# Kernel optimization log

Measured on AMD Instinct MI355X. Metric: run time of the kernel, lower is better.

## Reference

```python
import jax, jax.numpy as jnp
import numpy as np

B, L, D, H, S = 4, 4096, 1024, 16, 4
DH = D // H


def setup_inputs() -> dict:
    key = jax.random.key(0)
    ks = jax.random.split(key, 12)
    std = 0.02
    inp = {
        "x": jax.random.normal(ks[0], (B, L, D), jnp.float32),
        "scale_logits": jax.random.normal(ks[1], (S,), jnp.float32),
        "wq": jax.random.normal(ks[2], (D, D), jnp.float32) * std,
        "bq": jnp.zeros((D,), jnp.float32),
        "wk": jax.random.normal(ks[3], (D, D), jnp.float32) * std,
        "bk": jnp.zeros((D,), jnp.float32),
        "wv": jax.random.normal(ks[4], (D, D), jnp.float32) * std,
        "bv": jnp.zeros((D,), jnp.float32),
        "wo": jax.random.normal(ks[5], (D, D), jnp.float32) * std,
        "bo": jnp.zeros((D,), jnp.float32),
        "ws": jax.random.normal(ks[6], (S, D, D), jnp.float32) * std,  # per-scale Linear weights (out,in)
        "bs": jax.random.normal(ks[7], (S, D), jnp.float32) * std,
    }
    return inp


def reference(x, scale_logits, wq, bq, wk, bk, wv, bv, wo, bo, ws, bs):
    # q/k/v projections; kept flat (B,L,D) since the torch code re-flattens before scale proj
    qf = x @ wq.T + bq
    kf = x @ wk.T + bk
    vf = x @ wv.T + bv
    # per-scale linear projection, vectorized over scales: (B,S,L,D)
    sq = jnp.einsum('bld,sed->bsle', qf, ws) + bs[None, :, None, :]
    sk = jnp.einsum('bld,sed->bsle', kf, ws) + bs[None, :, None, :]
    sv = jnp.einsum('bld,sed->bsle', vf, ws) + bs[None, :, None, :]
    sq = sq.reshape(B, S, L, H, DH)
    sk = sk.reshape(B, S, L, H, DH)
    sv = sv.reshape(B, S, L, H, DH)
    # faithful to torch: matmul over last two dims of (B,L,H,dh) -> per-position
    # head-mixing scores of shape (B,S,L,H,H)
    scale = 1.0 / np.sqrt(DH).astype(np.float32)
    scores = jnp.einsum('bslhd,bslgd->bslhg', sq, sk) * scale
    attn = jax.nn.softmax(scores, axis=-1)
    out = jnp.einsum('bslhg,bslgd->bslhd', attn, sv)  # (B,S,L,H,DH)
    w = jax.nn.softmax(scale_logits, axis=0)  # (S,)
    combined = jnp.einsum('s,bslhd->blhd', w, out).reshape(B, L, D)
    return combined @ wo.T + bo
```

## Files before the change

kernel.cpp:

```cpp
#include <hip/hip_runtime.h>


typedef unsigned short u16;
typedef __attribute__((ext_vector_type(8))) short s16x8;
typedef __attribute__((ext_vector_type(8))) unsigned short u16x8;
typedef __attribute__((ext_vector_type(4))) float f32x4;

#define MM 16384
#define DDIM 1024
#define DDSQ 1048576ull

__device__ __forceinline__ u16 f2bf(float f) {
  unsigned u = __float_as_uint(f);
  u = (u + 0x7FFFu + ((u >> 16) & 1u)) >> 16;
  return (u16)u;
}
__device__ __forceinline__ float b2f(u16 b) {
  return __uint_as_float(((unsigned)b) << 16);
}
__device__ __forceinline__ void gload_lds16(const void* g, void* l) {
  __builtin_amdgcn_global_load_lds(
      (const __attribute__((address_space(1))) void*)g,
      (__attribute__((address_space(3))) void*)l, 16, 0, 0);
}

__global__ __launch_bounds__(256) void k_f32_to_bf16(
    const float* __restrict__ in, u16* __restrict__ out, int n4) {
  int i = blockIdx.x * 256 + threadIdx.x;
  if (i >= n4) return;
  float4 v = reinterpret_cast<const float4*>(in)[i];
  ushort4 o;
  o.x = f2bf(v.x); o.y = f2bf(v.y); o.z = f2bf(v.z); o.w = f2bf(v.w);
  reinterpret_cast<ushort4*>(out)[i] = o;
}

__global__ __launch_bounds__(256) void k_transpose_bf16(
    const float* __restrict__ wq, const float* __restrict__ wk,
    const float* __restrict__ wv, u16* __restrict__ out) {
  __shared__ float tile[32][33];
  const float* src = (blockIdx.z == 0) ? wq : (blockIdx.z == 1) ? wk : wv;
  u16* dst = out + (size_t)blockIdx.z * DDSQ;
  int tx = threadIdx.x, ty = threadIdx.y;
  int bx = blockIdx.x * 32, by = blockIdx.y * 32;
#pragma unroll
  for (int i = 0; i < 4; ++i)
    tile[ty + 8 * i][tx] = src[(size_t)(by + ty + 8 * i) * DDIM + bx + tx];
  __syncthreads();
#pragma unroll
  for (int i = 0; i < 4; ++i)
    dst[(size_t)(bx + ty + 8 * i) * DDIM + by + tx] = f2bf(tile[tx][ty + 8 * i]);
}

__global__ __launch_bounds__(256) void k_bias_fuse(
    const float* __restrict__ ws, const float* __restrict__ bq,
    const float* __restrict__ bk, const float* __restrict__ bv,
    const float* __restrict__ bs, float* __restrict__ bf) {
  int idx = blockIdx.y;
  int s = idx / 3, t = idx - s * 3;
  const float* bt = (t == 0) ? bq : (t == 1) ? bk : bv;
  int lane = threadIdx.x & 63, wid = threadIdx.x >> 6;
  int e = blockIdx.x * 4 + wid;
  const float* wr = ws + (size_t)s * DDSQ + (size_t)e * DDIM;
  float p = 0.f;
  for (int j = lane; j < DDIM; j += 64) p += wr[j] * bt[j];
#pragma unroll
  for (int off = 32; off > 0; off >>= 1) p += __shfl_xor(p, off);
  if (lane == 0) bf[idx * DDIM + e] = p + bs[s * DDIM + e];
}

template <typename OutT>
__global__ __launch_bounds__(256) void k_gemm_bt(
    const u16* __restrict__ A, const u16* __restrict__ B, OutT* __restrict__ C,
    const float* __restrict__ bias, int M, int N, int K,
    size_t za, size_t zb, size_t zc, size_t zbias, int zmode) {
  __shared__ u16 lds_a[128 * 32];
  __shared__ u16 lds_b[128 * 32];

  int z = blockIdx.x >> 3;
  int n_blk = blockIdx.x & 7;
  int m_blk = blockIdx.y;
  if (zmode == 1) { A += (size_t)(z / 3) * za; B += (size_t)(z % 3) * zb; }
  else            { A += (size_t)z * za;       B += (size_t)z * zb; }
  C += (size_t)z * zc;
  const float* biasz = bias ? (bias + (size_t)z * zbias) : nullptr;

  int m0 = m_blk * 128, n0 = n_blk * 128;
  int tid = threadIdx.x;
  int lane = tid & 63, wid = tid >> 6;
  int wm = wid >> 1, wn = wid & 1;

  f32x4 acc[4][4] = {};

  auto stage = [&](int k0) {
#pragma unroll
    for (int i = 0; i < 2; ++i) {
      int c = wid * 2 + i;
      int row = c * 16 + (lane >> 2);
      int col = (lane & 3) * 8;
      gload_lds16(A + (size_t)(m0 + row) * K + k0 + col, &lds_a[c * 512]);
      gload_lds16(B + (size_t)(n0 + row) * K + k0 + col, &lds_b[c * 512]);
    }
  };

  stage(0);
  int ar = (wm * 64 + (lane & 15)) * 32 + (lane >> 4) * 8;
  int br = (wn * 64 + (lane & 15)) * 32 + (lane >> 4) * 8;
  for (int k0 = 0;;) {
    __syncthreads();
    s16x8 af[4], bfr[4];
#pragma unroll
    for (int mi = 0; mi < 4; ++mi)
      af[mi] = *reinterpret_cast<const s16x8*>(&lds_a[ar + mi * 16 * 32]);
#pragma unroll
    for (int ni = 0; ni < 4; ++ni)
      bfr[ni] = *reinterpret_cast<const s16x8*>(&lds_b[br + ni * 16 * 32]);
#pragma unroll
    for (int mi = 0; mi < 4; ++mi)
#pragma unroll
      for (int ni = 0; ni < 4; ++ni)
        acc[mi][ni] = __builtin_amdgcn_mfma_f32_16x16x32_bf16(
            af[mi], bfr[ni], acc[mi][ni], 0, 0, 0);
    k0 += 32;
    if (k0 >= K) break;
    __syncthreads();
    stage(k0);
  }

#pragma unroll
  for (int mi = 0; mi < 4; ++mi) {
#pragma unroll
    for (int ni = 0; ni < 4; ++ni) {
      int colg = n0 + wn * 64 + ni * 16 + (lane & 15);
      float badd = biasz ? biasz[colg] : 0.f;
#pragma unroll
      for (int r = 0; r < 4; ++r) {
        int rowg = m0 + wm * 64 + mi * 16 + ((lane >> 4) << 2) + r;
        float v = acc[mi][ni][r] + badd;
        if constexpr (sizeof(OutT) == 2) C[(size_t)rowg * N + colg] = f2bf(v);
        else                             C[(size_t)rowg * N + colg] = v;
      }
    }
  }
}

template <typename OutT>
__global__ __launch_bounds__(512, 1) void k_gemm256(
    const u16* __restrict__ A, const u16* __restrict__ B, OutT* __restrict__ C,
    const float* __restrict__ bias, int M, int N, int K,
    size_t za, size_t zb, size_t zc, size_t zbias, int nbx) {
  __shared__ u16 lds[4][2][8192];

  int z = blockIdx.x / nbx;
  int nb = blockIdx.x - z * nbx;
  const u16* Ag = A + (size_t)z * za;
  const u16* Bg = B + (size_t)z * zb;
  OutT* Cg = C + (size_t)z * zc;
  const float* biasz = bias + (size_t)z * zbias;

  int m0 = blockIdx.y * 256, n0 = nb * 256;
  int tid = threadIdx.x;
  int lane = tid & 63, wid = tid >> 6;
  int wm = wid >> 2, wn = wid & 3;
  int NT = K >> 5;

  int scb = ((lane & 3) * 16) ^ (((lane >> 3) & 3) << 4);
  const char* srcA[2]; const char* srcB[2]; int ldsc[2];
#pragma unroll
  for (int r = 0; r < 2; ++r) {
    int c = r * 8 + wid;
    int row = c * 16 + (lane >> 2);
    srcA[r] = (const char*)Ag + ((size_t)(m0 + row) * K) * 2 + scb;
    srcB[r] = (const char*)Bg + ((size_t)(n0 + row) * K) * 2 + scb;
    ldsc[r] = c * 1024;
  }
  char* lbase = (char*)&lds[0][0][0];

  int fxor = ((lane >> 4) * 16) ^ (((lane >> 1) & 3) << 4);
  int aoff = (wm * 128 + (lane & 15)) * 64 + fxor;
  int boff = (wn * 64 + (lane & 15)) * 64 + fxor;

  f32x4 acc[8][4] = {};
  s16x8 cA0[4], cA1[4], cB[4];
  s16x8 nA0[4], nA1[4], nB[4];

#define STAGE_A(kt, rg)                                                   \
  {                                                                       \
    _Pragma("unroll") for (int r = 0; r < 2; ++r)                         \
        gload_lds16(srcA[r] + (size_t)(kt) * 64,                          \
                    lbase + (rg) * 32768 + ldsc[r]);                      \
  }
#define STAGE_B(kt, rg)                                                   \
  {                                                                       \
    _Pragma("unroll") for (int r = 0; r < 2; ++r)                         \
        gload_lds16(srcB[r] + (size_t)(kt) * 64,                          \
                    lbase + (rg) * 32768 + 16384 + ldsc[r]);              \
  }

#define SUBITER(C0, C1, CBv, N0, N1, NBv, tcur)                           \
  {                                                                       \
    asm volatile("s_waitcnt vmcnt(4)" ::: "memory");                      \
    asm volatile("s_barrier" ::: "memory");                               \
    int tn = (tcur) + 1 < NT ? (tcur) + 1 : NT - 1;                       \
    const char* bA = lbase + (tn & 3) * 32768;                            \
    const char* bB = bA + 16384;                                          \
    _Pragma("unroll") for (int i = 0; i < 4; ++i)                         \
        NBv[i] = *(const s16x8*)(bB + boff + i * 1024);                   \
    _Pragma("unroll") for (int i = 0; i < 4; ++i)                         \
        N0[i] = *(const s16x8*)(bA + aoff + i * 1024);                    \
    _Pragma("unroll") for (int i = 0; i < 4; ++i)                         \
        N1[i] = *(const s16x8*)(bA + aoff + 4096 + i * 1024);             \
    int ts = (tcur) + 3 < NT ? (tcur) + 3 : NT - 1;                       \
    int rgs = ((tcur) + 3) & 3;                                           \
    STAGE_A(ts, rgs); STAGE_B(ts, rgs);                                   \
    __builtin_amdgcn_s_setprio(1);                                        \
    _Pragma("unroll") for (int mi = 0; mi < 4; ++mi)                      \
      _Pragma("unroll") for (int ni = 0; ni < 4; ++ni)                    \
          acc[mi][ni] = __builtin_amdgcn_mfma_f32_16x16x32_bf16(          \
              C0[mi], CBv[ni], acc[mi][ni], 0, 0, 0);                     \
    _Pragma("unroll") for (int mi = 0; mi < 4; ++mi)                      \
      _Pragma("unroll") for (int ni = 0; ni < 4; ++ni)                    \
          acc[mi + 4][ni] = __builtin_amdgcn_mfma_f32_16x16x32_bf16(      \
              C1[mi], CBv[ni], acc[mi + 4][ni], 0, 0, 0);                 \
    __builtin_amdgcn_s_setprio(0);                                        \
  }

  STAGE_A(0, 0); STAGE_B(0, 0);
  STAGE_A(1, 1); STAGE_B(1, 1);
  STAGE_A(2, 2); STAGE_B(2, 2);
  asm volatile("s_waitcnt vmcnt(8)" ::: "memory");
  asm volatile("s_barrier" ::: "memory");
  {
    const char* bA = lbase;
    const char* bB = bA + 16384;
#pragma unroll
    for (int i = 0; i < 4; ++i) cB[i]  = *(const s16x8*)(bB + boff + i * 1024);
#pragma unroll
    for (int i = 0; i < 4; ++i) cA0[i] = *(const s16x8*)(bA + aoff + i * 1024);
#pragma unroll
    for (int i = 0; i < 4; ++i)
      cA1[i] = *(const s16x8*)(bA + aoff + 4096 + i * 1024);
  }

  for (int t = 0; t < NT; t += 2) {
    SUBITER(cA0, cA1, cB, nA0, nA1, nB, t);
    SUBITER(nA0, nA1, nB, cA0, cA1, cB, t + 1);
  }
#undef SUBITER
#undef STAGE_A
#undef STAGE_B

  asm volatile("s_waitcnt vmcnt(0)" ::: "memory");

#pragma unroll
  for (int mi = 0; mi < 8; ++mi) {
#pragma unroll
    for (int ni = 0; ni < 4; ++ni) {
      int colg = n0 + wn * 64 + ni * 16 + (lane & 15);
      float badd = biasz[colg];
#pragma unroll
      for (int r = 0; r < 4; ++r) {
        int rowg = m0 + wm * 128 + mi * 16 + ((lane >> 4) << 2) + r;
        float v = acc[mi][ni][r] + badd;
        if constexpr (sizeof(OutT) == 2) Cg[(size_t)rowg * N + colg] = f2bf(v);
        else                             Cg[(size_t)rowg * N + colg] = v;
      }
    }
  }
}

__global__ __launch_bounds__(256) void k_attn_all(
    const u16* __restrict__ proj, u16* __restrict__ outbf,
    const float* __restrict__ sl, int rows) {
  __shared__ u16 kv[4][2][1024];
  int lane = threadIdx.x & 63, wid = threadIdx.x >> 6;
  int row = blockIdx.x * 4 + wid;
  int h = lane >> 2, dq = lane & 3;
  int doff = h * 64 + dq * 16;

  float l0 = sl[0], l1 = sl[1], l2 = sl[2], l3 = sl[3];
  float lm = fmaxf(fmaxf(l0, l1), fmaxf(l2, l3));
  float e0 = __expf(l0 - lm), e1 = __expf(l1 - lm), e2 = __expf(l2 - lm),
        e3 = __expf(l3 - lm);
  float esum = e0 + e1 + e2 + e3;
  float wsc4[4] = {e0 / esum, e1 / esum, e2 / esum, e3 / esum};

  float acc[16];
#pragma unroll
  for (int i = 0; i < 16; ++i) acc[i] = 0.f;

  for (int s = 0; s < 4; ++s) {
    const u16* kr = proj + ((size_t)(3 * s + 1) * rows + row) * DDIM;
    const u16* vr = proj + ((size_t)(3 * s + 2) * rows + row) * DDIM;
    asm volatile("s_waitcnt vmcnt(0) lgkmcnt(0)" ::: "memory");
    gload_lds16(kr + lane * 8,       &kv[wid][0][0]);
    gload_lds16(kr + 512 + lane * 8, &kv[wid][0][512]);
    gload_lds16(vr + lane * 8,       &kv[wid][1][0]);
    gload_lds16(vr + 512 + lane * 8, &kv[wid][1][512]);

    const u16* qr = proj + ((size_t)(3 * s) * rows + row) * DDIM + doff;
    u16x8 q0 = *reinterpret_cast<const u16x8*>(qr);
    u16x8 q1 = *reinterpret_cast<const u16x8*>(qr + 8);
    float qf[16];
#pragma unroll
    for (int i = 0; i < 8; ++i) {
      qf[i]     = b2f(q0[i]) * 0.125f;
      qf[8 + i] = b2f(q1[i]) * 0.125f;
    }
    asm volatile("s_waitcnt vmcnt(0)" ::: "memory");

    float sc[16];
#pragma unroll
    for (int g = 0; g < 16; ++g) {
      const u16* kp = &kv[wid][0][g * 64 + dq * 16];
      u16x8 k0 = *reinterpret_cast<const u16x8*>(kp);
      u16x8 k1 = *reinterpret_cast<const u16x8*>(kp + 8);
      float d = 0.f;
#pragma unroll
      for (int i = 0; i < 8; ++i) d = fmaf(qf[i], b2f(k0[i]), d);
#pragma unroll
      for (int i = 0; i < 8; ++i) d = fmaf(qf[8 + i], b2f(k1[i]), d);
      d += __shfl_xor(d, 1);
      d += __shfl_xor(d, 2);
      sc[g] = d;
    }

    float mx = sc[0];
#pragma unroll
    for (int g = 1; g < 16; ++g) mx = fmaxf(mx, sc[g]);
    float sum = 0.f;
#pragma unroll
    for (int g = 0; g < 16; ++g) { sc[g] = __expf(sc[g] - mx); sum += sc[g]; }
    float inv = wsc4[s] / sum;
#pragma unroll
    for (int g = 0; g < 16; ++g) sc[g] *= inv;

#pragma unroll
    for (int g = 0; g < 16; ++g) {
      float a = sc[g];
      const u16* vp = &kv[wid][1][g * 64 + dq * 16];
      u16x8 v0 = *reinterpret_cast<const u16x8*>(vp);
      u16x8 v1 = *reinterpret_cast<const u16x8*>(vp + 8);
#pragma unroll
      for (int i = 0; i < 8; ++i) {
        acc[i]     = fmaf(a, b2f(v0[i]), acc[i]);
        acc[8 + i] = fmaf(a, b2f(v1[i]), acc[8 + i]);
      }
    }
  }

  u16* op = outbf + (size_t)row * DDIM + doff;
  u16x8 o0, o1;
#pragma unroll
  for (int i = 0; i < 8; ++i) {
    o0[i] = f2bf(acc[i]);
    o1[i] = f2bf(acc[8 + i]);
  }
  *reinterpret_cast<u16x8*>(op) = o0;
  *reinterpret_cast<u16x8*>(op + 8) = o1;
}

extern "C" void kernel_launch(void* const* d_in, const int* in_sizes, int n_in,
                              void* d_out, int out_size, void* d_ws,
                              size_t ws_size, hipStream_t stream) {
  const float* x  = (const float*)d_in[0];
  const float* sl = (const float*)d_in[1];
  const float* wq = (const float*)d_in[2];
  const float* bq = (const float*)d_in[3];
  const float* wk = (const float*)d_in[4];
  const float* bk = (const float*)d_in[5];
  const float* wv = (const float*)d_in[6];
  const float* bv = (const float*)d_in[7];
  const float* wo = (const float*)d_in[8];
  const float* bo = (const float*)d_in[9];
  const float* ws = (const float*)d_in[10];
  const float* bs = (const float*)d_in[11];
  float* out = (float*)d_out;

  char* wsb = (char*)d_ws;
  size_t off = 0;
  u16* xbf    = (u16*)(wsb + off); off += (size_t)MM * DDIM * 2;
  u16* wfus   = (u16*)(wsb + off); off += 12ull * DDSQ * 2;
  u16* wobf   = (u16*)(wsb + off); off += DDSQ * 2;
  float* bfus = (float*)(wsb + off); off += 65536;
  u16* combc  = (u16*)(wsb + off); off += (size_t)MM * DDIM * 2;
  char* dynr  = wsb + off;
  size_t fixed = off;

  int chunk = 4096;
  while (chunk > 1024 && fixed + (size_t)12 * chunk * DDIM * 2 > ws_size)
    chunk >>= 1;
  u16* projc = (u16*)dynr;
  u16* wtT  = (u16*)dynr;
  u16* wsbf = (u16*)(dynr + 3ull * DDSQ * 2);

  int n4;
  n4 = MM * DDIM / 4;
  k_f32_to_bf16<<<(n4 + 255) / 256, 256, 0, stream>>>(x, xbf, n4);
  n4 = (int)(4 * DDSQ / 4);
  k_f32_to_bf16<<<(n4 + 255) / 256, 256, 0, stream>>>(ws, wsbf, n4);
  n4 = (int)(DDSQ / 4);
  k_f32_to_bf16<<<(n4 + 255) / 256, 256, 0, stream>>>(wo, wobf, n4);

  k_transpose_bf16<<<dim3(32, 32, 3), dim3(32, 8), 0, stream>>>(wq, wk, wv, wtT);
  k_bias_fuse<<<dim3(256, 12), 256, 0, stream>>>(ws, bq, bk, bv, bs, bfus);

  k_gemm_bt<u16><<<dim3(96, 8), 256, 0, stream>>>(
      wsbf, wtT, wfus, nullptr, 1024, 1024, 1024, DDSQ, DDSQ, DDSQ, 0, 1);

  int nchunks = MM / chunk;
  for (int c = 0; c < nchunks; ++c) {
    const u16* xa = xbf + (size_t)c * chunk * DDIM;
    k_gemm256<u16><<<dim3(48, chunk / 256), 512, 0, stream>>>(
        xa, wfus, projc, bfus, chunk, 1024, 1024,
        0, DDSQ, (size_t)chunk * DDIM, DDIM, 4);
    k_attn_all<<<dim3(chunk / 4), 256, 0, stream>>>(
        projc, combc + (size_t)c * chunk * DDIM, sl, chunk);
  }

  k_gemm256<float><<<dim3(4, 64), 512, 0, stream>>>(
      combc, wobf, out, bo, MM, 1024, 1024, 0, 0, 0, 0, 4);
}
```

Baseline: 717.9 us.

## Double-buffer QKV loads in attention, replace small GEMM, tune MFMA scheduling

The per-row attention kernel now stages q, k and v for two scales into a double-buffered LDS area and prefetches the next scales while computing the current one, instead of a full wait per scale with q read straight from global memory. The weight-fusion GEMM moves from the simple 128-tile kernel to the pipelined 256-tile kernel through a new zmode argument. In that kernel, s_setprio is replaced by sched_group_barrier hints that interleave MFMA, VMEM and LDS reads. The attention LDS footprint grows threefold, which may lower occupancy.

```diff
diff --git a/kernel.cpp b/kernel.cpp
--- a/kernel.cpp
+++ b/kernel.cpp
@@ -69,93 +69,19 @@
 }
 
 template <typename OutT>
-__global__ __launch_bounds__(256) void k_gemm_bt(
-    const u16* __restrict__ A, const u16* __restrict__ B, OutT* __restrict__ C,
-    const float* __restrict__ bias, int M, int N, int K,
-    size_t za, size_t zb, size_t zc, size_t zbias, int zmode) {
-  __shared__ u16 lds_a[128 * 32];
-  __shared__ u16 lds_b[128 * 32];
-
-  int z = blockIdx.x >> 3;
-  int n_blk = blockIdx.x & 7;
-  int m_blk = blockIdx.y;
-  if (zmode == 1) { A += (size_t)(z / 3) * za; B += (size_t)(z % 3) * zb; }
-  else            { A += (size_t)z * za;       B += (size_t)z * zb; }
-  C += (size_t)z * zc;
-  const float* biasz = bias ? (bias + (size_t)z * zbias) : nullptr;
-
-  int m0 = m_blk * 128, n0 = n_blk * 128;
-  int tid = threadIdx.x;
-  int lane = tid & 63, wid = tid >> 6;
-  int wm = wid >> 1, wn = wid & 1;
-
-  f32x4 acc[4][4] = {};
-
-  auto stage = [&](int k0) {
-#pragma unroll
-    for (int i = 0; i < 2; ++i) {
-      int c = wid * 2 + i;
-      int row = c * 16 + (lane >> 2);
-      int col = (lane & 3) * 8;
-      gload_lds16(A + (size_t)(m0 + row) * K + k0 + col, &lds_a[c * 512]);
-      gload_lds16(B + (size_t)(n0 + row) * K + k0 + col, &lds_b[c * 512]);
-    }
-  };
-
-  stage(0);
-  int ar = (wm * 64 + (lane & 15)) * 32 + (lane >> 4) * 8;
-  int br = (wn * 64 + (lane & 15)) * 32 + (lane >> 4) * 8;
-  for (int k0 = 0;;) {
-    __syncthreads();
-    s16x8 af[4], bfr[4];
-#pragma unroll
-    for (int mi = 0; mi < 4; ++mi)
-      af[mi] = *reinterpret_cast<const s16x8*>(&lds_a[ar + mi * 16 * 32]);
-#pragma unroll
-    for (int ni = 0; ni < 4; ++ni)
-      bfr[ni] = *reinterpret_cast<const s16x8*>(&lds_b[br + ni * 16 * 32]);
-#pragma unroll
-    for (int mi = 0; mi < 4; ++mi)
-#pragma unroll
-      for (int ni = 0; ni < 4; ++ni)
-        acc[mi][ni] = __builtin_amdgcn_mfma_f32_16x16x32_bf16(
-            af[mi], bfr[ni], acc[mi][ni], 0, 0, 0);
-    k0 += 32;
-    if (k0 >= K) break;
-    __syncthreads();
-    stage(k0);
-  }
-
-#pragma unroll
-  for (int mi = 0; mi < 4; ++mi) {
-#pragma unroll
-    for (int ni = 0; ni < 4; ++ni) {
-      int colg = n0 + wn * 64 + ni * 16 + (lane & 15);
-      float badd = biasz ? biasz[colg] : 0.f;
-#pragma unroll
-      for (int r = 0; r < 4; ++r) {
-        int rowg = m0 + wm * 64 + mi * 16 + ((lane >> 4) << 2) + r;
-        float v = acc[mi][ni][r] + badd;
-        if constexpr (sizeof(OutT) == 2) C[(size_t)rowg * N + colg] = f2bf(v);
-        else                             C[(size_t)rowg * N + colg] = v;
-      }
-    }
-  }
-}
-
-template <typename OutT>
 __global__ __launch_bounds__(512, 1) void k_gemm256(
     const u16* __restrict__ A, const u16* __restrict__ B, OutT* __restrict__ C,
     const float* __restrict__ bias, int M, int N, int K,
-    size_t za, size_t zb, size_t zc, size_t zbias, int nbx) {
+    size_t za, size_t zb, size_t zc, size_t zbias, int nbx, int zmode) {
   __shared__ u16 lds[4][2][8192];
 
   int z = blockIdx.x / nbx;
   int nb = blockIdx.x - z * nbx;
-  const u16* Ag = A + (size_t)z * za;
-  const u16* Bg = B + (size_t)z * zb;
+  const u16* Ag; const u16* Bg;
+  if (zmode == 1) { Ag = A + (size_t)(z / 3) * za; Bg = B + (size_t)(z % 3) * zb; }
+  else            { Ag = A + (size_t)z * za;       Bg = B + (size_t)z * zb; }
   OutT* Cg = C + (size_t)z * zc;
-  const float* biasz = bias + (size_t)z * zbias;
+  const float* biasz = bias ? (bias + (size_t)z * zbias) : nullptr;
 
   int m0 = blockIdx.y * 256, n0 = nb * 256;
   int tid = threadIdx.x;
@@ -212,7 +138,6 @@
     int ts = (tcur) + 3 < NT ? (tcur) + 3 : NT - 1;                       \
     int rgs = ((tcur) + 3) & 3;                                           \
     STAGE_A(ts, rgs); STAGE_B(ts, rgs);                                   \
-    __builtin_amdgcn_s_setprio(1);                                        \
     _Pragma("unroll") for (int mi = 0; mi < 4; ++mi)                      \
       _Pragma("unroll") for (int ni = 0; ni < 4; ++ni)                    \
           acc[mi][ni] = __builtin_amdgcn_mfma_f32_16x16x32_bf16(          \
@@ -221,7 +146,11 @@
       _Pragma("unroll") for (int ni = 0; ni < 4; ++ni)                    \
           acc[mi + 4][ni] = __builtin_amdgcn_mfma_f32_16x16x32_bf16(      \
               C1[mi], CBv[ni], acc[mi + 4][ni], 0, 0, 0);                 \
-    __builtin_amdgcn_s_setprio(0);                                        \
+    _Pragma("unroll") for (int g = 0; g < 4; ++g) {                       \
+      __builtin_amdgcn_sched_group_barrier(0x100, 3, 0);     \
+      __builtin_amdgcn_sched_group_barrier(0x010, 1, 0);     \
+      __builtin_amdgcn_sched_group_barrier(0x008, 8, 0);     \
+    }                                                                     \
   }
 
   STAGE_A(0, 0); STAGE_B(0, 0);
@@ -256,7 +185,7 @@
 #pragma unroll
     for (int ni = 0; ni < 4; ++ni) {
       int colg = n0 + wn * 64 + ni * 16 + (lane & 15);
-      float badd = biasz[colg];
+      float badd = biasz ? biasz[colg] : 0.f;
 #pragma unroll
       for (int r = 0; r < 4; ++r) {
         int rowg = m0 + wm * 128 + mi * 16 + ((lane >> 4) << 2) + r;
@@ -271,7 +200,7 @@
 __global__ __launch_bounds__(256) void k_attn_all(
     const u16* __restrict__ proj, u16* __restrict__ outbf,
     const float* __restrict__ sl, int rows) {
-  __shared__ u16 kv[4][2][1024];
+  __shared__ u16 kvq[4][2][3][1024];
   int lane = threadIdx.x & 63, wid = threadIdx.x >> 6;
   int row = blockIdx.x * 4 + wid;
   int h = lane >> 2, dq = lane & 3;
@@ -283,35 +212,47 @@
         e3 = __expf(l3 - lm);
   float esum = e0 + e1 + e2 + e3;
   float wsc4[4] = {e0 / esum, e1 / esum, e2 / esum, e3 / esum};
+  asm volatile("" ::: "memory");
+
+#define QKV_ISSUE(s, buf)                                                  \
+  {                                                                        \
+    const u16* qr = proj + ((size_t)(3 * (s) + 0) * rows + row) * DDIM;    \
+    const u16* kr = proj + ((size_t)(3 * (s) + 1) * rows + row) * DDIM;    \
+    const u16* vr = proj + ((size_t)(3 * (s) + 2) * rows + row) * DDIM;    \
+    gload_lds16(qr + lane * 8,       &kvq[wid][buf][0][0]);                \
+    gload_lds16(qr + 512 + lane * 8, &kvq[wid][buf][0][512]);              \
+    gload_lds16(kr + lane * 8,       &kvq[wid][buf][1][0]);                \
+    gload_lds16(kr + 512 + lane * 8, &kvq[wid][buf][1][512]);              \
+    gload_lds16(vr + lane * 8,       &kvq[wid][buf][2][0]);                \
+    gload_lds16(vr + 512 + lane * 8, &kvq[wid][buf][2][512]);              \
+  }
+
+  QKV_ISSUE(0, 0);
+  QKV_ISSUE(1, 1);
 
   float acc[16];
 #pragma unroll
   for (int i = 0; i < 16; ++i) acc[i] = 0.f;
 
+#pragma unroll
   for (int s = 0; s < 4; ++s) {
-    const u16* kr = proj + ((size_t)(3 * s + 1) * rows + row) * DDIM;
-    const u16* vr = proj + ((size_t)(3 * s + 2) * rows + row) * DDIM;
-    asm volatile("s_waitcnt vmcnt(0) lgkmcnt(0)" ::: "memory");
-    gload_lds16(kr + lane * 8,       &kv[wid][0][0]);
-    gload_lds16(kr + 512 + lane * 8, &kv[wid][0][512]);
-    gload_lds16(vr + lane * 8,       &kv[wid][1][0]);
-    gload_lds16(vr + 512 + lane * 8, &kv[wid][1][512]);
-
-    const u16* qr = proj + ((size_t)(3 * s) * rows + row) * DDIM + doff;
-    u16x8 q0 = *reinterpret_cast<const u16x8*>(qr);
-    u16x8 q1 = *reinterpret_cast<const u16x8*>(qr + 8);
+    if (s == 3) asm volatile("s_waitcnt vmcnt(0)" ::: "memory");
+    else        asm volatile("s_waitcnt vmcnt(6)" ::: "memory");
+
+    const u16* qp = &kvq[wid][s & 1][0][doff];
+    u16x8 q0 = *reinterpret_cast<const u16x8*>(qp);
+    u16x8 q1 = *reinterpret_cast<const u16x8*>(qp + 8);
     float qf[16];
 #pragma unroll
     for (int i = 0; i < 8; ++i) {
       qf[i]     = b2f(q0[i]) * 0.125f;
       qf[8 + i] = b2f(q1[i]) * 0.125f;
     }
-    asm volatile("s_waitcnt vmcnt(0)" ::: "memory");
 
     float sc[16];
 #pragma unroll
     for (int g = 0; g < 16; ++g) {
-      const u16* kp = &kv[wid][0][g * 64 + dq * 16];
+      const u16* kp = &kvq[wid][s & 1][1][g * 64 + dq * 16];
       u16x8 k0 = *reinterpret_cast<const u16x8*>(kp);
       u16x8 k1 = *reinterpret_cast<const u16x8*>(kp + 8);
       float d = 0.f;
@@ -337,7 +278,7 @@
 #pragma unroll
     for (int g = 0; g < 16; ++g) {
       float a = sc[g];
-      const u16* vp = &kv[wid][1][g * 64 + dq * 16];
+      const u16* vp = &kvq[wid][s & 1][2][g * 64 + dq * 16];
       u16x8 v0 = *reinterpret_cast<const u16x8*>(vp);
       u16x8 v1 = *reinterpret_cast<const u16x8*>(vp + 8);
 #pragma unroll
@@ -346,7 +287,14 @@
         acc[8 + i] = fmaf(a, b2f(v1[i]), acc[8 + i]);
       }
     }
-  }
+
+    if (s < 2) {
+      asm volatile("s_waitcnt lgkmcnt(0)" ::: "memory");
+      __builtin_amdgcn_sched_barrier(0);
+      QKV_ISSUE(s + 2, s & 1);
+    }
+  }
+#undef QKV_ISSUE
 
   u16* op = outbf + (size_t)row * DDIM + doff;
   u16x8 o0, o1;
@@ -404,19 +352,19 @@
   k_transpose_bf16<<<dim3(32, 32, 3), dim3(32, 8), 0, stream>>>(wq, wk, wv, wtT);
   k_bias_fuse<<<dim3(256, 12), 256, 0, stream>>>(ws, bq, bk, bv, bs, bfus);
 
-  k_gemm_bt<u16><<<dim3(96, 8), 256, 0, stream>>>(
-      wsbf, wtT, wfus, nullptr, 1024, 1024, 1024, DDSQ, DDSQ, DDSQ, 0, 1);
+  k_gemm256<u16><<<dim3(48, 4), 512, 0, stream>>>(
+      wsbf, wtT, wfus, nullptr, 1024, 1024, 1024, DDSQ, DDSQ, DDSQ, 0, 4, 1);
 
   int nchunks = MM / chunk;
   for (int c = 0; c < nchunks; ++c) {
     const u16* xa = xbf + (size_t)c * chunk * DDIM;
     k_gemm256<u16><<<dim3(48, chunk / 256), 512, 0, stream>>>(
         xa, wfus, projc, bfus, chunk, 1024, 1024,
-        0, DDSQ, (size_t)chunk * DDIM, DDIM, 4);
+        0, DDSQ, (size_t)chunk * DDIM, DDIM, 4, 0);
     k_attn_all<<<dim3(chunk / 4), 256, 0, stream>>>(
         projc, combc + (size_t)c * chunk * DDIM, sl, chunk);
   }
 
   k_gemm256<float><<<dim3(4, 64), 512, 0, stream>>>(
-      combc, wobf, out, bo, MM, 1024, 1024, 0, 0, 0, 0, 4);
-}
+      combc, wobf, out, bo, MM, 1024, 1024, 0, 0, 0, 0, 4, 0);
+}
```

Measured after the change: 1.075 ms. 49.7% more time.

## Add 32x32x16 MFMA GEMM with direct-global B fragments for fused projection

Applied to the files above, without the earlier changes.

Introduces a new GEMM kernel for the big fused x·W projection that uses 32x32x16 bf16 MFMA instructions instead of 16x16 tiles. Only A tiles are staged through LDS in a 4-deep ring. B fragments are loaded straight from global memory into registers and double-buffered across k-steps. The intent is to cut LDS traffic and instruction count per FLOP and raise occupancy with launch_bounds(512,2). The risks are uncoalesced or latency-bound direct B loads, and the lack of any LDS swizzle, which could cause bank conflicts on the A reads.

```diff
diff --git a/kernel.cpp b/kernel.cpp
--- a/kernel.cpp
+++ b/kernel.cpp
@@ -5,6 +5,7 @@
 typedef __attribute__((ext_vector_type(8))) short s16x8;
 typedef __attribute__((ext_vector_type(8))) unsigned short u16x8;
 typedef __attribute__((ext_vector_type(4))) float f32x4;
+typedef __attribute__((ext_vector_type(16))) float f32x16;
 
 #define MM 16384
 #define DDIM 1024
@@ -195,7 +196,6 @@
         gload_lds16(srcB[r] + (size_t)(kt) * 64,                          \
                     lbase + (rg) * 32768 + 16384 + ldsc[r]);              \
   }
-
 #define SUBITER(C0, C1, CBv, N0, N1, NBv, tcur)                           \
   {                                                                       \
     asm volatile("s_waitcnt vmcnt(4)" ::: "memory");                      \
@@ -268,6 +268,111 @@
   }
 }
 
+__global__ __launch_bounds__(512, 2) void k_gemm32(
+    const u16* __restrict__ A, const u16* __restrict__ B, u16* __restrict__ C,
+    const float* __restrict__ bias, int M, int N, int K,
+    size_t za, size_t zb, size_t zc, size_t zbias, int nbx) {
+  __shared__ char lds[4 * 16384];
+
+  int z = blockIdx.x / nbx;
+  int nb = blockIdx.x - z * nbx;
+  const u16* Ag = A + (size_t)z * za;
+  const u16* Bg = B + (size_t)z * zb;
+  u16* Cg = C + (size_t)z * zc;
+  const float* biasz = bias + (size_t)z * zbias;
+
+  int m0 = blockIdx.y * 256, n0 = nb * 256;
+  int tid = threadIdx.x;
+  int lane = tid & 63, wid = tid >> 6;
+  int wm = wid >> 2, wn = wid & 3;
+  int NT = K >> 5;
+  int lrow = lane & 31, lhalf = lane >> 5;
+
+  const char* srcA[2];
+#pragma unroll
+  for (int i = 0; i < 2; ++i)
+    srcA[i] = (const char*)Ag +
+              ((size_t)(m0 + wid * 32 + lrow) * K + i * 16 + lhalf * 8) * 2;
+
+  const char* pB[2];
+#pragma unroll
+  for (int nf = 0; nf < 2; ++nf)
+    pB[nf] = (const char*)Bg +
+             ((size_t)(n0 + wn * 64 + nf * 32 + lrow) * K + lhalf * 8) * 2;
+
+  char* lb = lds;
+  int lane16 = lane * 16;
+
+  f32x16 acc[4][2] = {};
+  s16x8 cBf[2][2], nBf[2][2];
+
+#define STAGE_A(kt, rg)                                                   \
+  {                                                                       \
+    _Pragma("unroll") for (int i = 0; i < 2; ++i)                         \
+        gload_lds16(srcA[i] + (size_t)(kt) * 64,                          \
+                    lb + (rg) * 16384 + (wid * 2 + i) * 1024);            \
+  }
+
+#define SUBITER(CB_, NB_, tcur)                                           \
+  {                                                                        \
+    asm volatile("s_waitcnt vmcnt(8)" ::: "memory");   \
+    asm volatile("s_barrier" ::: "memory");                                \
+    const char* bA = lb + ((tcur) & 3) * 16384;                            \
+    s16x8 fa[4][2];                                                        \
+    _Pragma("unroll") for (int mf = 0; mf < 4; ++mf)                       \
+      _Pragma("unroll") for (int kk = 0; kk < 2; ++kk)                     \
+          fa[mf][kk] = *(const s16x8*)(bA +                                \
+              ((wm * 4 + mf) * 2 + kk) * 1024 + lane16);                   \
+    int tn = (tcur) + 1 < NT ? (tcur) + 1 : NT - 1;                        \
+    _Pragma("unroll") for (int nf = 0; nf < 2; ++nf)                       \
+      _Pragma("unroll") for (int kk = 0; kk < 2; ++kk)                     \
+          NB_[nf][kk] = *(const s16x8*)(pB[nf] +                           \
+              (size_t)tn * 64 + kk * 32);                                  \
+    int ts = (tcur) + 3 < NT ? (tcur) + 3 : NT - 1;                        \
+    STAGE_A(ts, ((tcur) + 3) & 3);                                         \
+    __builtin_amdgcn_s_setprio(1);                                         \
+    _Pragma("unroll") for (int mf = 0; mf < 4; ++mf)                       \
+      _Pragma("unroll") for (int nf = 0; nf < 2; ++nf)                     \
+        _Pragma("unroll") for (int kk = 0; kk < 2; ++kk)                   \
+            acc[mf][nf] = __builtin_amdgcn_mfma_f32_32x32x16_bf16(         \
+                fa[mf][kk], CB_[nf][kk], acc[mf][nf], 0, 0, 0);            \
+    __builtin_amdgcn_s_setprio(0);                                         \
+  }
+
+  STAGE_A(0, 0);
+  STAGE_A(1, 1);
+  STAGE_A(2, 2);
+#pragma unroll
+  for (int nf = 0; nf < 2; ++nf)
+#pragma unroll
+    for (int kk = 0; kk < 2; ++kk)
+      cBf[nf][kk] = *(const s16x8*)(pB[nf] + kk * 32);
+
+  for (int t = 0; t < NT; t += 2) {
+    SUBITER(cBf, nBf, t);
+    SUBITER(nBf, cBf, t + 1);
+  }
+#undef SUBITER
+#undef STAGE_A
+
+  asm volatile("s_waitcnt vmcnt(0)" ::: "memory");
+
+#pragma unroll
+  for (int mf = 0; mf < 4; ++mf) {
+#pragma unroll
+    for (int nf = 0; nf < 2; ++nf) {
+      int colg = n0 + wn * 64 + nf * 32 + lrow;
+      float badd = biasz[colg];
+#pragma unroll
+      for (int reg = 0; reg < 16; ++reg) {
+        int rowf = (reg & 3) + 8 * (reg >> 2) + 4 * lhalf;
+        int rowg = m0 + wm * 128 + mf * 32 + rowf;
+        Cg[(size_t)rowg * N + colg] = f2bf(acc[mf][nf][reg] + badd);
+      }
+    }
+  }
+}
+
 __global__ __launch_bounds__(256) void k_attn_all(
     const u16* __restrict__ proj, u16* __restrict__ outbf,
     const float* __restrict__ sl, int rows) {
@@ -410,7 +515,7 @@
   int nchunks = MM / chunk;
   for (int c = 0; c < nchunks; ++c) {
     const u16* xa = xbf + (size_t)c * chunk * DDIM;
-    k_gemm256<u16><<<dim3(48, chunk / 256), 512, 0, stream>>>(
+    k_gemm32<<<dim3(48, chunk / 256), 512, 0, stream>>>(
         xa, wfus, projc, bfus, chunk, 1024, 1024,
         0, DDSQ, (size_t)chunk * DDIM, DDIM, 4);
     k_attn_all<<<dim3(chunk / 4), 256, 0, stream>>>(
```

New measurement: 1.015 ms. 1.41x slower.
